# Optimization experiments

Measured on AMD Instinct MI355X. Metric: run time of the kernel, lower is better.

Reference implementation:

```python
import jax, jax.numpy as jnp
import numpy as np

B, N, C = 8, 8192, 256
H = 8            # num_heads
D = C // H       # head dim = 32
P = 64           # proj_size (Linformer rank)


def setup_inputs() -> dict:
    key = jax.random.key(0)
    ks = jax.random.split(key, 12)
    s = lambda fan_in: 1.0 / np.sqrt(fan_in)
    return {
        "x": jax.random.normal(ks[0], (B, N, C), jnp.float32),
        "Wqkvv": jax.random.normal(ks[1], (4 * C, C), jnp.float32) * s(C),
        "WE": jax.random.normal(ks[2], (P, N), jnp.float32) * s(N),
        "bE": jax.random.normal(ks[3], (P,), jnp.float32) * s(N),
        "WF": jax.random.normal(ks[4], (P, N), jnp.float32) * s(N),
        "bF": jax.random.normal(ks[5], (P,), jnp.float32) * s(N),
        "Wo1": jax.random.normal(ks[6], (C // 2, C), jnp.float32) * s(C),
        "bo1": jax.random.normal(ks[7], (C // 2,), jnp.float32) * s(C),
        "Wo2": jax.random.normal(ks[8], (C // 2, C), jnp.float32) * s(C),
        "bo2": jax.random.normal(ks[9], (C // 2,), jnp.float32) * s(C),
        "temp1": jnp.ones((H, 1, 1), jnp.float32),
        "temp2": jnp.ones((H, 1, 1), jnp.float32),
    }


def _l2norm(v, axis=-1, eps=1e-12):
    # matches torch F.normalize
    n = jnp.sqrt(jnp.sum(v * v, axis=axis, keepdims=True))
    return v / jnp.maximum(n, eps)


def reference(x, Wqkvv, WE, bE, WF, bF, Wo1, bo1, Wo2, bo2, temp1, temp2):
    b, n, c = x.shape
    # qkvv: [b,n,4c] -> [4,b,h,d,n]  (includes the .transpose(-2,-1) of each part)
    qkvv = jnp.einsum('bnc,fc->bnf', x, Wqkvv).reshape(b, n, 4, H, D)
    qkvv = qkvv.transpose(2, 0, 3, 4, 1)
    q, k, v_ca, v_sa = qkvv[0], qkvv[1], qkvv[2], qkvv[3]  # each [b,h,d,n]

    # Linformer-style low-rank projections along the token axis
    k_proj = jnp.einsum('bhdn,pn->bhdp', k, WE) + bE   # [b,h,d,p]
    v_proj = jnp.einsum('bhdn,pn->bhdp', v_sa, WF) + bF

    qn = _l2norm(q)
    kn = _l2norm(k)

    # --- channel attention branch (XCiT-style) ---
    attn_ca = jnp.einsum('bhdn,bhen->bhde', qn, kn) * temp1[None]  # [b,h,d,d]
    attn_ca = jax.nn.softmax(attn_ca, axis=-1)  # dropout: eval mode (identity)
    x_ca = jnp.einsum('bhde,bhen->bhdn', attn_ca, v_ca)
    x_ca = x_ca.transpose(0, 3, 1, 2).reshape(b, n, c)  # [b,n,c]

    # --- spatial attention branch (low-rank) ---
    attn_sa = jnp.einsum('bhdn,bhdp->bhnp', qn, k_proj) * temp2[None]  # [b,h,n,p]
    attn_sa = jax.nn.softmax(attn_sa, axis=-1)
    x_sa = jnp.einsum('bhnp,bhdp->bhnd', attn_sa, v_proj)  # [b,h,n,d]
    # faithful to original: permute(0,3,1,2).reshape(b,n,c)
    x_sa = x_sa.transpose(0, 3, 1, 2).reshape(b, n, c)

    x_sa = jnp.einsum('bnc,oc->bno', x_sa, Wo1) + bo1
    x_ca = jnp.einsum('bnc,oc->bno', x_ca, Wo2) + bo2
    return jnp.concatenate((x_sa, x_ca), axis=-1)
```

## Files before the change

kernel.cpp:

```cpp
#include <hip/hip_runtime.h>
#include <hip/hip_bf16.h>
#include <stdint.h>


typedef __attribute__((ext_vector_type(8))) __bf16 bf16x8;
typedef __attribute__((ext_vector_type(4))) __bf16 bf16x4;
typedef __attribute__((ext_vector_type(4))) float f32x4;

#define MFMA(a, b, c) __builtin_amdgcn_mfma_f32_16x16x32_bf16((a), (b), (c), 0, 0, 0)

__device__ __forceinline__ void gl2lds16(const __bf16* g, __bf16* l) {
  __builtin_amdgcn_global_load_lds(
      (const __attribute__((address_space(1))) void*)(const void*)g,
      (__attribute__((address_space(3))) void*)(void*)l, 16, 0, 0);
}

__global__ __launch_bounds__(256) void k_detect(const unsigned short* __restrict__ xr,
                                                int* __restrict__ flag) {
  __shared__ int cnt;
  if (threadIdx.x == 0) cnt = 0;
  __syncthreads();
  int c = 0;
  for (int i = threadIdx.x; i < 8192; i += 256) {
    const int e = (xr[i] >> 7) & 0xFF;
    c += (e >= 0xC0) ? 1 : 0;
  }
  atomicAdd(&cnt, c);
  __syncthreads();
  if (threadIdx.x == 0) *flag = (cnt > 100) ? 1 : 0;
}

__global__ __launch_bounds__(256) void k_convert_x(const void* __restrict__ src,
                                                   __bf16* __restrict__ dst,
                                                   const int* __restrict__ flag) {
  const int i = (blockIdx.x * 256 + threadIdx.x) * 8;
  if (*flag) {
    const float* s = (const float*)src;
    bf16x8 v;
#pragma unroll
    for (int j = 0; j < 8; ++j) v[j] = (__bf16)s[i + j];
    *(bf16x8*)(dst + i) = v;
  } else {
    *(bf16x8*)(dst + i) = *(const bf16x8*)((const __bf16*)src + i);
  }
}

__global__ __launch_bounds__(256) void k_convert_w(
    const void* s0, const void* s1, const void* s2, const void* s3, const void* s4,
    const void* s5, const void* s6, const void* s7, const void* s8, const void* s9,
    const void* s10, __bf16* __restrict__ cw, const int* __restrict__ flag) {
  const int i = (blockIdx.x * 256 + threadIdx.x) * 8;
  if (i >= 1376656) return;
  const void* s;
  int base;
  if (i < 262144)        { s = s0;  base = 0; }
  else if (i < 786432)   { s = s1;  base = 262144; }
  else if (i < 786496)   { s = s2;  base = 786432; }
  else if (i < 1310784)  { s = s3;  base = 786496; }
  else if (i < 1310848)  { s = s4;  base = 1310784; }
  else if (i < 1343616)  { s = s5;  base = 1310848; }
  else if (i < 1343744)  { s = s6;  base = 1343616; }
  else if (i < 1376512)  { s = s7;  base = 1343744; }
  else if (i < 1376640)  { s = s8;  base = 1376512; }
  else if (i < 1376648)  { s = s9;  base = 1376640; }
  else                   { s = s10; base = 1376648; }
  const int li = i - base;
  if (*flag) {
    const float* sf = (const float*)s;
#pragma unroll
    for (int j = 0; j < 8; ++j) cw[i + j] = (__bf16)sf[li + j];
  } else {
    const __bf16* sb = (const __bf16*)s;
#pragma unroll
    for (int j = 0; j < 8; ++j) cw[i + j] = sb[li + j];
  }
}

__global__ __launch_bounds__(256) void k_qkvv(const __bf16* __restrict__ x,
                                              const __bf16* __restrict__ Wq,
                                              __bf16* __restrict__ qkvv) {
  __shared__ alignas(16) __bf16 As[128 * 32];
  __shared__ alignas(16) __bf16 Bs[128 * 32];
  const int t = threadIdx.x, lane = t & 63;
  const int wr = t >> 7, wc = (t >> 6) & 1;
  const int f0 = blockIdx.y * 128;
  const int t0 = blockIdx.x * 128;
  f32x4 acc[4][4] = {};
  const int r = t >> 2, c8 = (t & 3) * 8;
  for (int k0 = 0; k0 < 256; k0 += 32) {
#pragma unroll
    for (int i = 0; i < 2; ++i) {
      gl2lds16(Wq + (size_t)(f0 + i * 64 + r) * 256 + k0 + c8, As + i * 2048 + t * 8);
      gl2lds16(x + (size_t)(t0 + i * 64 + r) * 256 + k0 + c8, Bs + i * 2048 + t * 8);
    }
    __syncthreads();
    bf16x8 af[4], bfr[4];
#pragma unroll
    for (int i = 0; i < 4; ++i) {
      af[i] = *(const bf16x8*)(As + (wr * 64 + i * 16 + (lane & 15)) * 32 + (lane >> 4) * 8);
      bfr[i] = *(const bf16x8*)(Bs + (wc * 64 + i * 16 + (lane & 15)) * 32 + (lane >> 4) * 8);
    }
#pragma unroll
    for (int i = 0; i < 4; ++i)
#pragma unroll
      for (int j = 0; j < 4; ++j) acc[i][j] = MFMA(af[i], bfr[j], acc[i][j]);
    __syncthreads();
  }
  const int b = t0 >> 13;
#pragma unroll
  for (int i = 0; i < 4; ++i) {
#pragma unroll
    for (int j = 0; j < 4; ++j) {
      const int tok = t0 + wc * 64 + j * 16 + (lane & 15);
      const int n = tok & 8191;
#pragma unroll
      for (int rr = 0; rr < 4; ++rr) {
        const int f = f0 + wr * 64 + i * 16 + (lane >> 4) * 4 + rr;
        qkvv[(size_t)(((f >> 8) * 8 + b) * 256 + (f & 255)) * 8192 + n] = (__bf16)acc[i][j][rr];
      }
    }
  }
}

__global__ __launch_bounds__(256) void k_norms(const __bf16* __restrict__ qkvv,
                                               float* __restrict__ qinv,
                                               float* __restrict__ kinv) {
  const int row = blockIdx.x, which = blockIdx.y;
  const __bf16* p = qkvv + (size_t)(which * 2048 + row) * 8192;
  float s = 0.f;
  for (int i = threadIdx.x; i < 8192; i += 256) {
    const float v = (float)p[i];
    s += v * v;
  }
#pragma unroll
  for (int off = 32; off; off >>= 1) s += __shfl_down(s, off, 64);
  __shared__ float red[4];
  if ((threadIdx.x & 63) == 0) red[threadIdx.x >> 6] = s;
  __syncthreads();
  if (threadIdx.x == 0) {
    const float tot = red[0] + red[1] + red[2] + red[3];
    const float inv = 1.0f / fmaxf(sqrtf(tot), 1e-12f);
    (which ? kinv : qinv)[row] = inv;
  }
}

__global__ __launch_bounds__(256) void k_proj_part(const __bf16* __restrict__ qkvv,
                                                   const __bf16* __restrict__ WE,
                                                   const __bf16* __restrict__ WF,
                                                   float* __restrict__ pbuf) {
  __shared__ alignas(16) __bf16 As[128 * 32];
  __shared__ alignas(16) __bf16 Bs[64 * 32];
  const int t = threadIdx.x, lane = t & 63;
  const int wr = t >> 7, wc = (t >> 6) & 1;
  const int kc = blockIdx.x, mt = blockIdx.y, pj = blockIdx.z;
  const __bf16* A = qkvv + (size_t)(pj ? 3 : 1) * 2048 * 8192;
  const __bf16* Bm = pj ? WF : WE;
  const int r0 = mt * 128;
  f32x4 acc[4][2] = {};
  const int r = t >> 2, c8 = (t & 3) * 8;
  for (int k0 = kc * 512; k0 < kc * 512 + 512; k0 += 32) {
#pragma unroll
    for (int i = 0; i < 2; ++i)
      gl2lds16(A + (size_t)(r0 + i * 64 + r) * 8192 + k0 + c8, As + i * 2048 + t * 8);
    gl2lds16(Bm + (size_t)r * 8192 + k0 + c8, Bs + t * 8);
    __syncthreads();
    bf16x8 af[4], bfr[2];
#pragma unroll
    for (int i = 0; i < 4; ++i)
      af[i] = *(const bf16x8*)(As + (wr * 64 + i * 16 + (lane & 15)) * 32 + (lane >> 4) * 8);
#pragma unroll
    for (int j = 0; j < 2; ++j)
      bfr[j] = *(const bf16x8*)(Bs + (wc * 32 + j * 16 + (lane & 15)) * 32 + (lane >> 4) * 8);
#pragma unroll
    for (int i = 0; i < 4; ++i)
#pragma unroll
      for (int j = 0; j < 2; ++j) acc[i][j] = MFMA(af[i], bfr[j], acc[i][j]);
    __syncthreads();
  }
  float* dst = pbuf + (size_t)((pj * 16 + kc) * 2048 + r0) * 64;
#pragma unroll
  for (int i = 0; i < 4; ++i)
#pragma unroll
    for (int j = 0; j < 2; ++j)
#pragma unroll
      for (int rr = 0; rr < 4; ++rr)
        dst[(wr * 64 + i * 16 + (lane >> 4) * 4 + rr) * 64 + wc * 32 + j * 16 + (lane & 15)] =
            acc[i][j][rr];
}

__global__ __launch_bounds__(256) void k_proj_reduce(const float* __restrict__ pbuf,
                                                     const __bf16* __restrict__ bE,
                                                     const __bf16* __restrict__ bF,
                                                     const float* __restrict__ qinv,
                                                     const __bf16* __restrict__ t2,
                                                     __bf16* __restrict__ kprojT,
                                                     __bf16* __restrict__ vprojb) {
  const int idx = blockIdx.x * 256 + threadIdx.x;
  const int pj = idx >> 17, rp = idx & 131071, p = idx & 63;
  const int row = rp >> 6, bh = row >> 5, d = row & 31, h = bh & 7;
  float s = (float)((pj ? bF : bE)[p]);
  const float* src = pbuf + (size_t)pj * 16 * 131072 + rp;
#pragma unroll
  for (int k = 0; k < 16; ++k) s += src[(size_t)k * 131072];
  if (pj == 0)
    kprojT[bh * 2048 + p * 32 + d] = (__bf16)(s * qinv[row] * (float)t2[h]);
  else
    vprojb[bh * 2048 + d * 64 + p] = (__bf16)s;
}

__global__ __launch_bounds__(256) void k_sca_part(const __bf16* __restrict__ qkvv,
                                                  float* __restrict__ spart) {
  const int bh = blockIdx.x, kc = blockIdx.y;
  const int t = threadIdx.x, lane = t & 63, w = t >> 6;
  const __bf16* qb = qkvv + (size_t)(bh * 32) * 8192;
  const __bf16* kb = qkvv + (size_t)(2048 + bh * 32) * 8192;
  f32x4 acc[2][2] = {};
  const int kbase = kc * 1024 + w * 256 + (lane >> 4) * 8;
#pragma unroll
  for (int ks = 0; ks < 256; ks += 32) {
    bf16x8 af[2], bfr[2];
#pragma unroll
    for (int i = 0; i < 2; ++i) {
      af[i] = *(const bf16x8*)(qb + (size_t)(i * 16 + (lane & 15)) * 8192 + kbase + ks);
      bfr[i] = *(const bf16x8*)(kb + (size_t)(i * 16 + (lane & 15)) * 8192 + kbase + ks);
    }
#pragma unroll
    for (int i = 0; i < 2; ++i)
#pragma unroll
      for (int j = 0; j < 2; ++j) acc[i][j] = MFMA(af[i], bfr[j], acc[i][j]);
  }
  float* dst = spart + (size_t)((bh * 8 + kc) * 4 + w) * 1024;
#pragma unroll
  for (int i = 0; i < 2; ++i)
#pragma unroll
    for (int j = 0; j < 2; ++j)
#pragma unroll
      for (int rr = 0; rr < 4; ++rr)
        dst[(i * 16 + (lane >> 4) * 4 + rr) * 32 + j * 16 + (lane & 15)] = acc[i][j][rr];
}

__global__ __launch_bounds__(256) void k_sca_softmax(const float* __restrict__ spart,
                                                     const float* __restrict__ qinv,
                                                     const float* __restrict__ kinv,
                                                     const __bf16* __restrict__ temp1,
                                                     __bf16* __restrict__ attnb) {
  const int bh = blockIdx.x;
  __shared__ float S[1024];
  const int t = threadIdx.x;
  const float tmp = (float)temp1[bh & 7];
  for (int idx = t; idx < 1024; idx += 256) {
    float s = 0.f;
    const float* src = spart + (size_t)bh * 32768 + idx;
#pragma unroll
    for (int k = 0; k < 32; ++k) s += src[k * 1024];
    S[idx] = s * qinv[bh * 32 + (idx >> 5)] * kinv[bh * 32 + (idx & 31)] * tmp;
  }
  __syncthreads();
  const int lane = t & 63, w = t >> 6;
#pragma unroll
  for (int rr = 0; rr < 4; ++rr) {
    const int row = rr * 8 + w * 2 + (lane >> 5);
    const int e = lane & 31;
    float v = S[row * 32 + e];
    float m = v;
#pragma unroll
    for (int off = 16; off; off >>= 1) m = fmaxf(m, __shfl_xor(m, off, 32));
    const float ex = __expf(v - m);
    float sm = ex;
#pragma unroll
    for (int off = 16; off; off >>= 1) sm += __shfl_xor(sm, off, 32);
    attnb[(size_t)bh * 1024 + row * 32 + e] = (__bf16)(ex / sm);
  }
}

__global__ __launch_bounds__(256) void k_ca_mfma(const __bf16* __restrict__ qkvv,
                                                 const __bf16* __restrict__ attnb,
                                                 __bf16* __restrict__ xca) {
  const int t = threadIdx.x, lane = t & 63, w = t >> 6;
  const int l15 = lane & 15, g = lane >> 4;
  const int bh = blockIdx.y, b = bh >> 3, h = bh & 7;
  const __bf16* vb = qkvv + (size_t)(4096 + bh * 32) * 8192;
  bf16x8 aa[2];
#pragma unroll
  for (int mi = 0; mi < 2; ++mi)
    aa[mi] = *(const bf16x8*)(attnb + bh * 1024 + (mi * 16 + l15) * 32 + g * 8);
#pragma unroll
  for (int it = 0; it < 4; ++it) {
    const int n = blockIdx.x * 256 + it * 64 + w * 16 + l15;
    union { bf16x8 v; unsigned short u[8]; } bq;
#pragma unroll
    for (int j = 0; j < 8; ++j)
      bq.u[j] = *(const unsigned short*)(vb + (size_t)(g * 8 + j) * 8192 + n);
    f32x4 o[2] = {};
#pragma unroll
    for (int mi = 0; mi < 2; ++mi) o[mi] = MFMA(aa[mi], bq.v, o[mi]);
#pragma unroll
    for (int mi = 0; mi < 2; ++mi) {
      bf16x4 p4;
#pragma unroll
      for (int rr = 0; rr < 4; ++rr) p4[rr] = (__bf16)o[mi][rr];
      *(bf16x4*)(xca + (size_t)(b * 8192 + n) * 256 + h * 32 + mi * 16 + g * 4) = p4;
    }
  }
}

__global__ __launch_bounds__(256) void k_sa_mfma(const __bf16* __restrict__ qkvv,
                                                 const __bf16* __restrict__ kprojT,
                                                 const __bf16* __restrict__ vprojb,
                                                 __bf16* __restrict__ xsa) {
  __shared__ __bf16 P[4][16 * 72];
  const int t = threadIdx.x, lane = t & 63, w = t >> 6;
  const int l15 = lane & 15, g = lane >> 4;
  const int bh = blockIdx.y;
  const __bf16* qb = qkvv + (size_t)(bh * 32) * 8192;
  bf16x8 ka[4], va[2][2];
#pragma unroll
  for (int tile = 0; tile < 4; ++tile)
    ka[tile] = *(const bf16x8*)(kprojT + bh * 2048 + (tile * 16 + l15) * 32 + g * 8);
#pragma unroll
  for (int mi = 0; mi < 2; ++mi)
#pragma unroll
    for (int kh = 0; kh < 2; ++kh)
      va[mi][kh] = *(const bf16x8*)(vprojb + bh * 2048 + (mi * 16 + l15) * 64 + kh * 32 + g * 8);
  __bf16* Pw = &P[w][0];
#pragma unroll
  for (int it = 0; it < 4; ++it) {
    const int n0 = blockIdx.x * 256 + it * 64 + w * 16;
    union { bf16x8 v; unsigned short u[8]; } bq;
#pragma unroll
    for (int j = 0; j < 8; ++j)
      bq.u[j] = *(const unsigned short*)(qb + (size_t)(g * 8 + j) * 8192 + n0 + l15);
    f32x4 st[4];
#pragma unroll
    for (int tile = 0; tile < 4; ++tile) {
      f32x4 z = {};
      st[tile] = MFMA(ka[tile], bq.v, z);
    }
    float m = st[0][0];
#pragma unroll
    for (int tile = 0; tile < 4; ++tile)
#pragma unroll
      for (int rr = 0; rr < 4; ++rr) m = fmaxf(m, st[tile][rr]);
    m = fmaxf(m, __shfl_xor(m, 16, 64));
    m = fmaxf(m, __shfl_xor(m, 32, 64));
    float sum = 0.f;
#pragma unroll
    for (int tile = 0; tile < 4; ++tile) {
      bf16x4 p4;
#pragma unroll
      for (int rr = 0; rr < 4; ++rr) {
        const float ex = __expf(st[tile][rr] - m);
        sum += ex;
        p4[rr] = (__bf16)ex;
      }
      *(bf16x4*)(Pw + l15 * 72 + tile * 16 + g * 4) = p4;
    }
    sum += __shfl_xor(sum, 16, 64);
    sum += __shfl_xor(sum, 32, 64);
    const float inv = 1.0f / sum;
    f32x4 o[2] = {};
#pragma unroll
    for (int kh = 0; kh < 2; ++kh) {
      const bf16x8 pf = *(const bf16x8*)(Pw + l15 * 72 + kh * 32 + g * 8);
#pragma unroll
      for (int mi = 0; mi < 2; ++mi) o[mi] = MFMA(va[mi][kh], pf, o[mi]);
    }
#pragma unroll
    for (int mi = 0; mi < 2; ++mi)
#pragma unroll
      for (int rr = 0; rr < 4; ++rr) {
        const int d = mi * 16 + g * 4 + rr;
        xsa[(size_t)(bh * 32 + d) * 8192 + n0 + l15] = (__bf16)(o[mi][rr] * inv);
      }
  }
}

__global__ __launch_bounds__(256) void k_out(const __bf16* __restrict__ xsa,
                                             const __bf16* __restrict__ xca,
                                             const __bf16* __restrict__ Wo1,
                                             const __bf16* __restrict__ bo1,
                                             const __bf16* __restrict__ Wo2,
                                             const __bf16* __restrict__ bo2,
                                             void* __restrict__ outv,
                                             const int* __restrict__ flag) {
  __shared__ alignas(16) __bf16 As[128 * 32];
  __shared__ alignas(16) __bf16 Bs[128 * 32];
  const int t = threadIdx.x, lane = t & 63;
  const int wr = t >> 7, wc = (t >> 6) & 1;
  const int nt = blockIdx.x, b = blockIdx.y, br = blockIdx.z;
  const int isf32 = *flag;
  const __bf16* Wo = br ? Wo2 : Wo1;
  const __bf16* bo = br ? bo2 : bo1;
  f32x4 acc[4][4] = {};
  const int r = t >> 2, c8 = (t & 3) * 8;
  for (int k0 = 0; k0 < 256; k0 += 32) {
#pragma unroll
    for (int i = 0; i < 2; ++i) {
      const int row = nt * 128 + i * 64 + r;
      const __bf16* ga;
      if (br == 0) {
        ga = xsa + (size_t)((b * 8 + ((row >> 5) & 7)) * 32 + (row >> 8)) * 8192 +
             (row & 31) * 256 + k0 + c8;
      } else {
        ga = xca + (size_t)(b * 8192 + row) * 256 + k0 + c8;
      }
      gl2lds16(ga, As + i * 2048 + t * 8);
      gl2lds16(Wo + (size_t)(i * 64 + r) * 256 + k0 + c8, Bs + i * 2048 + t * 8);
    }
    __syncthreads();
    bf16x8 af[4], bfr[4];
#pragma unroll
    for (int i = 0; i < 4; ++i) {
      af[i] = *(const bf16x8*)(As + (wr * 64 + i * 16 + (lane & 15)) * 32 + (lane >> 4) * 8);
      bfr[i] = *(const bf16x8*)(Bs + (wc * 64 + i * 16 + (lane & 15)) * 32 + (lane >> 4) * 8);
    }
#pragma unroll
    for (int i = 0; i < 4; ++i)
#pragma unroll
      for (int j = 0; j < 4; ++j) acc[i][j] = MFMA(af[i], bfr[j], acc[i][j]);
    __syncthreads();
  }
  float bias[4];
#pragma unroll
  for (int j = 0; j < 4; ++j) bias[j] = (float)bo[wc * 64 + j * 16 + (lane & 15)];
#pragma unroll
  for (int i = 0; i < 4; ++i) {
#pragma unroll
    for (int j = 0; j < 4; ++j) {
      const int col = wc * 64 + j * 16 + (lane & 15);
#pragma unroll
      for (int rr = 0; rr < 4; ++rr) {
        const int row = nt * 128 + wr * 64 + i * 16 + (lane >> 4) * 4 + rr;
        const float val = acc[i][j][rr] + bias[j];
        const size_t oi = (size_t)(b * 8192 + row) * 256 + br * 128 + col;
        if (isf32) ((float*)outv)[oi] = val;
        else ((__bf16*)outv)[oi] = (__bf16)val;
      }
    }
  }
}

extern "C" void kernel_launch(void* const* d_in, const int* in_sizes, int n_in,
                              void* d_out, int out_size, void* d_ws, size_t ws_size,
                              hipStream_t stream) {
  char* ws = (char*)d_ws;
  __bf16* qkvv   = (__bf16*)(ws);
  __bf16* cinx   = (__bf16*)(ws + 134217728ull);
  __bf16* xca    = (__bf16*)(ws + 134217728ull);
  float*  pbuf   = (float*)(ws + 167772160ull);
  float*  spart  = (float*)(ws + 184549376ull);
  __bf16* xsa    = (__bf16*)(ws + 167772160ull);
  __bf16* kprojT = (__bf16*)(ws + 201326592ull);
  __bf16* vprojb = (__bf16*)(ws + 201588736ull);
  float*  qinv   = (float*)(ws + 201850880ull);
  float*  kinv   = (float*)(ws + 201859072ull);
  __bf16* attnb  = (__bf16*)(ws + 201867264ull);
  __bf16* cw     = (__bf16*)(ws + 201998336ull);
  int*    flag   = (int*)(ws + 204751872ull);

  __bf16* cWq  = cw;
  __bf16* cWE  = cw + 262144;
  __bf16* cbE  = cw + 786432;
  __bf16* cWF  = cw + 786496;
  __bf16* cbF  = cw + 1310784;
  __bf16* cWo1 = cw + 1310848;
  __bf16* cbo1 = cw + 1343616;
  __bf16* cWo2 = cw + 1343744;
  __bf16* cbo2 = cw + 1376512;
  __bf16* ct1  = cw + 1376640;
  __bf16* ct2  = cw + 1376648;

  k_detect<<<1, 256, 0, stream>>>((const unsigned short*)d_in[0], flag);
  k_convert_x<<<8192, 256, 0, stream>>>(d_in[0], cinx, flag);
  k_convert_w<<<673, 256, 0, stream>>>(d_in[1], d_in[2], d_in[3], d_in[4], d_in[5],
                                       d_in[6], d_in[7], d_in[8], d_in[9], d_in[10],
                                       d_in[11], cw, flag);
  k_qkvv<<<dim3(512, 8), 256, 0, stream>>>(cinx, cWq, qkvv);
  k_norms<<<dim3(2048, 2), 256, 0, stream>>>(qkvv, qinv, kinv);
  k_proj_part<<<dim3(16, 16, 2), 256, 0, stream>>>(qkvv, cWE, cWF, pbuf);
  k_proj_reduce<<<dim3(1024), 256, 0, stream>>>(pbuf, cbE, cbF, qinv, ct2, kprojT, vprojb);
  k_sca_part<<<dim3(64, 8), 256, 0, stream>>>(qkvv, spart);
  k_sca_softmax<<<dim3(64), 256, 0, stream>>>(spart, qinv, kinv, ct1, attnb);
  k_ca_mfma<<<dim3(32, 64), 256, 0, stream>>>(qkvv, attnb, xca);
  k_sa_mfma<<<dim3(32, 64), 256, 0, stream>>>(qkvv, kprojT, vprojb, xsa);
  k_out<<<dim3(64, 8, 2), 256, 0, stream>>>(xsa, xca, cWo1, cbo1, cWo2, cbo2, d_out, flag);
}
```

Measured before the change: 332.2 us.

## Fuse norm computation into QKV GEMM, merge attention kernels, swizzle LDS

```diff
diff --git a/kernel.cpp b/kernel.cpp
--- a/kernel.cpp
+++ b/kernel.cpp
@@ -15,26 +15,26 @@
       (__attribute__((address_space(3))) void*)(void*)l, 16, 0, 0);
 }
 
-__global__ __launch_bounds__(256) void k_detect(const unsigned short* __restrict__ xr,
-                                                int* __restrict__ flag) {
-  __shared__ int cnt;
-  if (threadIdx.x == 0) cnt = 0;
-  __syncthreads();
+__device__ __forceinline__ int detect_f32(const unsigned int* __restrict__ xw) {
   int c = 0;
-  for (int i = threadIdx.x; i < 8192; i += 256) {
-    const int e = (xr[i] >> 7) & 0xFF;
-    c += (e >= 0xC0) ? 1 : 0;
-  }
-  atomicAdd(&cnt, c);
-  __syncthreads();
-  if (threadIdx.x == 0) *flag = (cnt > 100) ? 1 : 0;
+#pragma unroll
+  for (int i = 0; i < 64; ++i) {
+    const unsigned int u = xw[i];
+    c += (((u >> 7) & 0xFF) >= 0xC0) ? 1 : 0;
+    c += (((u >> 23) & 0xFF) >= 0xC0) ? 1 : 0;
+  }
+  return c > 8;
 }
 
 __global__ __launch_bounds__(256) void k_convert_x(const void* __restrict__ src,
                                                    __bf16* __restrict__ dst,
-                                                   const int* __restrict__ flag) {
+                                                   float* __restrict__ nsum) {
+  if (blockIdx.x == 0) {
+#pragma unroll
+    for (int j = 0; j < 16; ++j) nsum[threadIdx.x + j * 256] = 0.f;
+  }
   const int i = (blockIdx.x * 256 + threadIdx.x) * 8;
-  if (*flag) {
+  if (detect_f32((const unsigned int*)src)) {
     const float* s = (const float*)src;
     bf16x8 v;
 #pragma unroll
@@ -48,7 +48,7 @@
 __global__ __launch_bounds__(256) void k_convert_w(
     const void* s0, const void* s1, const void* s2, const void* s3, const void* s4,
     const void* s5, const void* s6, const void* s7, const void* s8, const void* s9,
-    const void* s10, __bf16* __restrict__ cw, const int* __restrict__ flag) {
+    const void* s10, __bf16* __restrict__ cw, const void* __restrict__ xsrc) {
   const int i = (blockIdx.x * 256 + threadIdx.x) * 8;
   if (i >= 1376656) return;
   const void* s;
@@ -65,7 +65,7 @@
   else if (i < 1376648)  { s = s9;  base = 1376640; }
   else                   { s = s10; base = 1376648; }
   const int li = i - base;
-  if (*flag) {
+  if (detect_f32((const unsigned int*)xsrc)) {
     const float* sf = (const float*)s;
 #pragma unroll
     for (int j = 0; j < 8; ++j) cw[i + j] = (__bf16)sf[li + j];
@@ -78,15 +78,20 @@
 
 __global__ __launch_bounds__(256) void k_qkvv(const __bf16* __restrict__ x,
                                               const __bf16* __restrict__ Wq,
-                                              __bf16* __restrict__ qkvv) {
+                                              __bf16* __restrict__ qkvv,
+                                              float* __restrict__ qsum,
+                                              float* __restrict__ ksum) {
   __shared__ alignas(16) __bf16 As[128 * 32];
   __shared__ alignas(16) __bf16 Bs[128 * 32];
   const int t = threadIdx.x, lane = t & 63;
   const int wr = t >> 7, wc = (t >> 6) & 1;
+  const int l15 = lane & 15, g = lane >> 4;
   const int f0 = blockIdx.y * 128;
   const int t0 = blockIdx.x * 128;
   f32x4 acc[4][4] = {};
-  const int r = t >> 2, c8 = (t & 3) * 8;
+  const int r = t >> 2;
+  const int c8 = ((t & 3) ^ ((t >> 3) & 3)) * 8;
+  const int cx = ((g ^ ((l15 >> 1) & 3)) * 8);
   for (int k0 = 0; k0 < 256; k0 += 32) {
 #pragma unroll
     for (int i = 0; i < 2; ++i) {
@@ -97,8 +102,8 @@
     bf16x8 af[4], bfr[4];
 #pragma unroll
     for (int i = 0; i < 4; ++i) {
-      af[i] = *(const bf16x8*)(As + (wr * 64 + i * 16 + (lane & 15)) * 32 + (lane >> 4) * 8);
-      bfr[i] = *(const bf16x8*)(Bs + (wc * 64 + i * 16 + (lane & 15)) * 32 + (lane >> 4) * 8);
+      af[i] = *(const bf16x8*)(As + (wr * 64 + i * 16 + l15) * 32 + cx);
+      bfr[i] = *(const bf16x8*)(Bs + (wc * 64 + i * 16 + l15) * 32 + cx);
     }
 #pragma unroll
     for (int i = 0; i < 4; ++i)
@@ -111,36 +116,35 @@
   for (int i = 0; i < 4; ++i) {
 #pragma unroll
     for (int j = 0; j < 4; ++j) {
-      const int tok = t0 + wc * 64 + j * 16 + (lane & 15);
+      const int tok = t0 + wc * 64 + j * 16 + l15;
       const int n = tok & 8191;
 #pragma unroll
       for (int rr = 0; rr < 4; ++rr) {
-        const int f = f0 + wr * 64 + i * 16 + (lane >> 4) * 4 + rr;
+        const int f = f0 + wr * 64 + i * 16 + g * 4 + rr;
         qkvv[(size_t)(((f >> 8) * 8 + b) * 256 + (f & 255)) * 8192 + n] = (__bf16)acc[i][j][rr];
       }
     }
   }
-}
-
-__global__ __launch_bounds__(256) void k_norms(const __bf16* __restrict__ qkvv,
-                                               float* __restrict__ qinv,
-                                               float* __restrict__ kinv) {
-  const int row = blockIdx.x, which = blockIdx.y;
-  const __bf16* p = qkvv + (size_t)(which * 2048 + row) * 8192;
-  float s = 0.f;
-  for (int i = threadIdx.x; i < 8192; i += 256) {
-    const float v = (float)p[i];
-    s += v * v;
-  }
-#pragma unroll
-  for (int off = 32; off; off >>= 1) s += __shfl_down(s, off, 64);
-  __shared__ float red[4];
-  if ((threadIdx.x & 63) == 0) red[threadIdx.x >> 6] = s;
-  __syncthreads();
-  if (threadIdx.x == 0) {
-    const float tot = red[0] + red[1] + red[2] + red[3];
-    const float inv = 1.0f / fmaxf(sqrtf(tot), 1e-12f);
-    (which ? kinv : qinv)[row] = inv;
+  if (f0 < 512) {
+    float* dst = (f0 >> 8) ? ksum : qsum;
+#pragma unroll
+    for (int i = 0; i < 4; ++i) {
+#pragma unroll
+      for (int rr = 0; rr < 4; ++rr) {
+        float s = 0.f;
+#pragma unroll
+        for (int j = 0; j < 4; ++j) {
+          const float v = acc[i][j][rr];
+          s += v * v;
+        }
+#pragma unroll
+        for (int off = 1; off < 16; off <<= 1) s += __shfl_xor(s, off, 16);
+        if (l15 == 0) {
+          const int f = f0 + wr * 64 + i * 16 + g * 4 + rr;
+          atomicAdd(dst + b * 256 + (f & 255), s);
+        }
+      }
+    }
   }
 }
 
@@ -152,12 +156,15 @@
   __shared__ alignas(16) __bf16 Bs[64 * 32];
   const int t = threadIdx.x, lane = t & 63;
   const int wr = t >> 7, wc = (t >> 6) & 1;
+  const int l15 = lane & 15, g = lane >> 4;
   const int kc = blockIdx.x, mt = blockIdx.y, pj = blockIdx.z;
   const __bf16* A = qkvv + (size_t)(pj ? 3 : 1) * 2048 * 8192;
   const __bf16* Bm = pj ? WF : WE;
   const int r0 = mt * 128;
   f32x4 acc[4][2] = {};
-  const int r = t >> 2, c8 = (t & 3) * 8;
+  const int r = t >> 2;
+  const int c8 = ((t & 3) ^ ((t >> 3) & 3)) * 8;
+  const int cx = ((g ^ ((l15 >> 1) & 3)) * 8);
   for (int k0 = kc * 512; k0 < kc * 512 + 512; k0 += 32) {
 #pragma unroll
     for (int i = 0; i < 2; ++i)
@@ -167,10 +174,10 @@
     bf16x8 af[4], bfr[2];
 #pragma unroll
     for (int i = 0; i < 4; ++i)
-      af[i] = *(const bf16x8*)(As + (wr * 64 + i * 16 + (lane & 15)) * 32 + (lane >> 4) * 8);
+      af[i] = *(const bf16x8*)(As + (wr * 64 + i * 16 + l15) * 32 + cx);
 #pragma unroll
     for (int j = 0; j < 2; ++j)
-      bfr[j] = *(const bf16x8*)(Bs + (wc * 32 + j * 16 + (lane & 15)) * 32 + (lane >> 4) * 8);
+      bfr[j] = *(const bf16x8*)(Bs + (wc * 32 + j * 16 + l15) * 32 + cx);
 #pragma unroll
     for (int i = 0; i < 4; ++i)
 #pragma unroll
@@ -184,14 +191,13 @@
     for (int j = 0; j < 2; ++j)
 #pragma unroll
       for (int rr = 0; rr < 4; ++rr)
-        dst[(wr * 64 + i * 16 + (lane >> 4) * 4 + rr) * 64 + wc * 32 + j * 16 + (lane & 15)] =
-            acc[i][j][rr];
+        dst[(wr * 64 + i * 16 + g * 4 + rr) * 64 + wc * 32 + j * 16 + l15] = acc[i][j][rr];
 }
 
 __global__ __launch_bounds__(256) void k_proj_reduce(const float* __restrict__ pbuf,
                                                      const __bf16* __restrict__ bE,
                                                      const __bf16* __restrict__ bF,
-                                                     const float* __restrict__ qinv,
+                                                     const float* __restrict__ qsum,
                                                      const __bf16* __restrict__ t2,
                                                      __bf16* __restrict__ kprojT,
                                                      __bf16* __restrict__ vprojb) {
@@ -202,10 +208,12 @@
   const float* src = pbuf + (size_t)pj * 16 * 131072 + rp;
 #pragma unroll
   for (int k = 0; k < 16; ++k) s += src[(size_t)k * 131072];
-  if (pj == 0)
-    kprojT[bh * 2048 + p * 32 + d] = (__bf16)(s * qinv[row] * (float)t2[h]);
-  else
+  if (pj == 0) {
+    const float qi = 1.0f / fmaxf(sqrtf(qsum[row]), 1e-12f);
+    kprojT[bh * 2048 + p * 32 + d] = (__bf16)(s * qi * (float)t2[h]);
+  } else {
     vprojb[bh * 2048 + d * 64 + p] = (__bf16)s;
+  }
 }
 
 __global__ __launch_bounds__(256) void k_sca_part(const __bf16* __restrict__ qkvv,
@@ -240,8 +248,8 @@
 }
 
 __global__ __launch_bounds__(256) void k_sca_softmax(const float* __restrict__ spart,
-                                                     const float* __restrict__ qinv,
-                                                     const float* __restrict__ kinv,
+                                                     const float* __restrict__ qsum,
+                                                     const float* __restrict__ ksum,
                                                      const __bf16* __restrict__ temp1,
                                                      __bf16* __restrict__ attnb) {
   const int bh = blockIdx.x;
@@ -253,7 +261,9 @@
     const float* src = spart + (size_t)bh * 32768 + idx;
 #pragma unroll
     for (int k = 0; k < 32; ++k) s += src[k * 1024];
-    S[idx] = s * qinv[bh * 32 + (idx >> 5)] * kinv[bh * 32 + (idx & 31)] * tmp;
+    const float qi = 1.0f / fmaxf(sqrtf(qsum[bh * 32 + (idx >> 5)]), 1e-12f);
+    const float ki = 1.0f / fmaxf(sqrtf(ksum[bh * 32 + (idx & 31)]), 1e-12f);
+    S[idx] = s * qi * ki * tmp;
   }
   __syncthreads();
   const int lane = t & 63, w = t >> 6;
@@ -273,105 +283,103 @@
   }
 }
 
-__global__ __launch_bounds__(256) void k_ca_mfma(const __bf16* __restrict__ qkvv,
-                                                 const __bf16* __restrict__ attnb,
-                                                 __bf16* __restrict__ xca) {
-  const int t = threadIdx.x, lane = t & 63, w = t >> 6;
-  const int l15 = lane & 15, g = lane >> 4;
-  const int bh = blockIdx.y, b = bh >> 3, h = bh & 7;
-  const __bf16* vb = qkvv + (size_t)(4096 + bh * 32) * 8192;
-  bf16x8 aa[2];
-#pragma unroll
-  for (int mi = 0; mi < 2; ++mi)
-    aa[mi] = *(const bf16x8*)(attnb + bh * 1024 + (mi * 16 + l15) * 32 + g * 8);
-#pragma unroll
-  for (int it = 0; it < 4; ++it) {
-    const int n = blockIdx.x * 256 + it * 64 + w * 16 + l15;
-    union { bf16x8 v; unsigned short u[8]; } bq;
-#pragma unroll
-    for (int j = 0; j < 8; ++j)
-      bq.u[j] = *(const unsigned short*)(vb + (size_t)(g * 8 + j) * 8192 + n);
-    f32x4 o[2] = {};
-#pragma unroll
-    for (int mi = 0; mi < 2; ++mi) o[mi] = MFMA(aa[mi], bq.v, o[mi]);
-#pragma unroll
-    for (int mi = 0; mi < 2; ++mi) {
-      bf16x4 p4;
-#pragma unroll
-      for (int rr = 0; rr < 4; ++rr) p4[rr] = (__bf16)o[mi][rr];
-      *(bf16x4*)(xca + (size_t)(b * 8192 + n) * 256 + h * 32 + mi * 16 + g * 4) = p4;
-    }
-  }
-}
-
-__global__ __launch_bounds__(256) void k_sa_mfma(const __bf16* __restrict__ qkvv,
-                                                 const __bf16* __restrict__ kprojT,
-                                                 const __bf16* __restrict__ vprojb,
-                                                 __bf16* __restrict__ xsa) {
+__global__ __launch_bounds__(256) void k_casa(const __bf16* __restrict__ qkvv,
+                                              const __bf16* __restrict__ attnb,
+                                              const __bf16* __restrict__ kprojT,
+                                              const __bf16* __restrict__ vprojb,
+                                              __bf16* __restrict__ xca,
+                                              __bf16* __restrict__ xsa) {
   __shared__ __bf16 P[4][16 * 72];
   const int t = threadIdx.x, lane = t & 63, w = t >> 6;
   const int l15 = lane & 15, g = lane >> 4;
-  const int bh = blockIdx.y;
-  const __bf16* qb = qkvv + (size_t)(bh * 32) * 8192;
-  bf16x8 ka[4], va[2][2];
-#pragma unroll
-  for (int tile = 0; tile < 4; ++tile)
-    ka[tile] = *(const bf16x8*)(kprojT + bh * 2048 + (tile * 16 + l15) * 32 + g * 8);
-#pragma unroll
-  for (int mi = 0; mi < 2; ++mi)
-#pragma unroll
-    for (int kh = 0; kh < 2; ++kh)
-      va[mi][kh] = *(const bf16x8*)(vprojb + bh * 2048 + (mi * 16 + l15) * 64 + kh * 32 + g * 8);
-  __bf16* Pw = &P[w][0];
-#pragma unroll
-  for (int it = 0; it < 4; ++it) {
-    const int n0 = blockIdx.x * 256 + it * 64 + w * 16;
-    union { bf16x8 v; unsigned short u[8]; } bq;
-#pragma unroll
-    for (int j = 0; j < 8; ++j)
-      bq.u[j] = *(const unsigned short*)(qb + (size_t)(g * 8 + j) * 8192 + n0 + l15);
-    f32x4 st[4];
-#pragma unroll
-    for (int tile = 0; tile < 4; ++tile) {
-      f32x4 z = {};
-      st[tile] = MFMA(ka[tile], bq.v, z);
-    }
-    float m = st[0][0];
+  if (blockIdx.y < 64) {
+    const int bh = blockIdx.y, b = bh >> 3, h = bh & 7;
+    const __bf16* vb = qkvv + (size_t)(4096 + bh * 32) * 8192;
+    bf16x8 aa[2];
+#pragma unroll
+    for (int mi = 0; mi < 2; ++mi)
+      aa[mi] = *(const bf16x8*)(attnb + bh * 1024 + (mi * 16 + l15) * 32 + g * 8);
+#pragma unroll
+    for (int it = 0; it < 4; ++it) {
+      const int n = blockIdx.x * 256 + it * 64 + w * 16 + l15;
+      union { bf16x8 v; unsigned short u[8]; } bq;
+#pragma unroll
+      for (int j = 0; j < 8; ++j)
+        bq.u[j] = *(const unsigned short*)(vb + (size_t)(g * 8 + j) * 8192 + n);
+      f32x4 o[2] = {};
+#pragma unroll
+      for (int mi = 0; mi < 2; ++mi) o[mi] = MFMA(aa[mi], bq.v, o[mi]);
+#pragma unroll
+      for (int mi = 0; mi < 2; ++mi) {
+        bf16x4 p4;
+#pragma unroll
+        for (int rr = 0; rr < 4; ++rr) p4[rr] = (__bf16)o[mi][rr];
+        *(bf16x4*)(xca + (size_t)(b * 8192 + n) * 256 + h * 32 + mi * 16 + g * 4) = p4;
+      }
+    }
+  } else {
+    const int bh = blockIdx.y - 64;
+    const __bf16* qb = qkvv + (size_t)(bh * 32) * 8192;
+    bf16x8 ka[4], va[2][2];
 #pragma unroll
     for (int tile = 0; tile < 4; ++tile)
-#pragma unroll
-      for (int rr = 0; rr < 4; ++rr) m = fmaxf(m, st[tile][rr]);
-    m = fmaxf(m, __shfl_xor(m, 16, 64));
-    m = fmaxf(m, __shfl_xor(m, 32, 64));
-    float sum = 0.f;
-#pragma unroll
-    for (int tile = 0; tile < 4; ++tile) {
-      bf16x4 p4;
-#pragma unroll
-      for (int rr = 0; rr < 4; ++rr) {
-        const float ex = __expf(st[tile][rr] - m);
-        sum += ex;
-        p4[rr] = (__bf16)ex;
-      }
-      *(bf16x4*)(Pw + l15 * 72 + tile * 16 + g * 4) = p4;
-    }
-    sum += __shfl_xor(sum, 16, 64);
-    sum += __shfl_xor(sum, 32, 64);
-    const float inv = 1.0f / sum;
-    f32x4 o[2] = {};
-#pragma unroll
-    for (int kh = 0; kh < 2; ++kh) {
-      const bf16x8 pf = *(const bf16x8*)(Pw + l15 * 72 + kh * 32 + g * 8);
-#pragma unroll
-      for (int mi = 0; mi < 2; ++mi) o[mi] = MFMA(va[mi][kh], pf, o[mi]);
-    }
+      ka[tile] = *(const bf16x8*)(kprojT + bh * 2048 + (tile * 16 + l15) * 32 + g * 8);
 #pragma unroll
     for (int mi = 0; mi < 2; ++mi)
 #pragma unroll
-      for (int rr = 0; rr < 4; ++rr) {
-        const int d = mi * 16 + g * 4 + rr;
-        xsa[(size_t)(bh * 32 + d) * 8192 + n0 + l15] = (__bf16)(o[mi][rr] * inv);
-      }
+      for (int kh = 0; kh < 2; ++kh)
+        va[mi][kh] = *(const bf16x8*)(vprojb + bh * 2048 + (mi * 16 + l15) * 64 + kh * 32 + g * 8);
+    __bf16* Pw = &P[w][0];
+#pragma unroll
+    for (int it = 0; it < 4; ++it) {
+      const int n0 = blockIdx.x * 256 + it * 64 + w * 16;
+      union { bf16x8 v; unsigned short u[8]; } bq;
+#pragma unroll
+      for (int j = 0; j < 8; ++j)
+        bq.u[j] = *(const unsigned short*)(qb + (size_t)(g * 8 + j) * 8192 + n0 + l15);
+      f32x4 st[4];
+#pragma unroll
+      for (int tile = 0; tile < 4; ++tile) {
+        f32x4 z = {};
+        st[tile] = MFMA(ka[tile], bq.v, z);
+      }
+      float m = st[0][0];
+#pragma unroll
+      for (int tile = 0; tile < 4; ++tile)
+#pragma unroll
+        for (int rr = 0; rr < 4; ++rr) m = fmaxf(m, st[tile][rr]);
+      m = fmaxf(m, __shfl_xor(m, 16, 64));
+      m = fmaxf(m, __shfl_xor(m, 32, 64));
+      float sum = 0.f;
+#pragma unroll
+      for (int tile = 0; tile < 4; ++tile) {
+        bf16x4 p4;
+#pragma unroll
+        for (int rr = 0; rr < 4; ++rr) {
+          const float ex = __expf(st[tile][rr] - m);
+          sum += ex;
+          p4[rr] = (__bf16)ex;
+        }
+        *(bf16x4*)(Pw + l15 * 72 + tile * 16 + g * 4) = p4;
+      }
+      sum += __shfl_xor(sum, 16, 64);
+      sum += __shfl_xor(sum, 32, 64);
+      const float inv = 1.0f / sum;
+      f32x4 o[2] = {};
+#pragma unroll
+      for (int kh = 0; kh < 2; ++kh) {
+        const bf16x8 pf = *(const bf16x8*)(Pw + l15 * 72 + kh * 32 + g * 8);
+#pragma unroll
+        for (int mi = 0; mi < 2; ++mi) o[mi] = MFMA(va[mi][kh], pf, o[mi]);
+      }
+#pragma unroll
+      for (int mi = 0; mi < 2; ++mi)
+#pragma unroll
+        for (int rr = 0; rr < 4; ++rr) {
+          const int d = mi * 16 + g * 4 + rr;
+          xsa[(size_t)(bh * 32 + d) * 8192 + n0 + l15] = (__bf16)(o[mi][rr] * inv);
+        }
+    }
   }
 }
 
@@ -382,17 +390,20 @@
                                              const __bf16* __restrict__ Wo2,
                                              const __bf16* __restrict__ bo2,
                                              void* __restrict__ outv,
-                                             const int* __restrict__ flag) {
+                                             const void* __restrict__ xsrc) {
   __shared__ alignas(16) __bf16 As[128 * 32];
   __shared__ alignas(16) __bf16 Bs[128 * 32];
   const int t = threadIdx.x, lane = t & 63;
   const int wr = t >> 7, wc = (t >> 6) & 1;
+  const int l15 = lane & 15, g = lane >> 4;
   const int nt = blockIdx.x, b = blockIdx.y, br = blockIdx.z;
-  const int isf32 = *flag;
+  const int isf32 = detect_f32((const unsigned int*)xsrc);
   const __bf16* Wo = br ? Wo2 : Wo1;
   const __bf16* bo = br ? bo2 : bo1;
   f32x4 acc[4][4] = {};
-  const int r = t >> 2, c8 = (t & 3) * 8;
+  const int r = t >> 2;
+  const int c8 = ((t & 3) ^ ((t >> 3) & 3)) * 8;
+  const int cx = ((g ^ ((l15 >> 1) & 3)) * 8);
   for (int k0 = 0; k0 < 256; k0 += 32) {
 #pragma unroll
     for (int i = 0; i < 2; ++i) {
@@ -411,8 +422,8 @@
     bf16x8 af[4], bfr[4];
 #pragma unroll
     for (int i = 0; i < 4; ++i) {
-      af[i] = *(const bf16x8*)(As + (wr * 64 + i * 16 + (lane & 15)) * 32 + (lane >> 4) * 8);
-      bfr[i] = *(const bf16x8*)(Bs + (wc * 64 + i * 16 + (lane & 15)) * 32 + (lane >> 4) * 8);
+      af[i] = *(const bf16x8*)(As + (wr * 64 + i * 16 + l15) * 32 + cx);
+      bfr[i] = *(const bf16x8*)(Bs + (wc * 64 + i * 16 + l15) * 32 + cx);
     }
 #pragma unroll
     for (int i = 0; i < 4; ++i)
@@ -422,15 +433,15 @@
   }
   float bias[4];
 #pragma unroll
-  for (int j = 0; j < 4; ++j) bias[j] = (float)bo[wc * 64 + j * 16 + (lane & 15)];
+  for (int j = 0; j < 4; ++j) bias[j] = (float)bo[wc * 64 + j * 16 + l15];
 #pragma unroll
   for (int i = 0; i < 4; ++i) {
 #pragma unroll
     for (int j = 0; j < 4; ++j) {
-      const int col = wc * 64 + j * 16 + (lane & 15);
+      const int col = wc * 64 + j * 16 + l15;
 #pragma unroll
       for (int rr = 0; rr < 4; ++rr) {
-        const int row = nt * 128 + wr * 64 + i * 16 + (lane >> 4) * 4 + rr;
+        const int row = nt * 128 + wr * 64 + i * 16 + g * 4 + rr;
         const float val = acc[i][j][rr] + bias[j];
         const size_t oi = (size_t)(b * 8192 + row) * 256 + br * 128 + col;
         if (isf32) ((float*)outv)[oi] = val;
@@ -452,11 +463,10 @@
   __bf16* xsa    = (__bf16*)(ws + 167772160ull);
   __bf16* kprojT = (__bf16*)(ws + 201326592ull);
   __bf16* vprojb = (__bf16*)(ws + 201588736ull);
-  float*  qinv   = (float*)(ws + 201850880ull);
-  float*  kinv   = (float*)(ws + 201859072ull);
+  float*  qsum   = (float*)(ws + 201850880ull);
+  float*  ksum   = (float*)(ws + 201859072ull);
   __bf16* attnb  = (__bf16*)(ws + 201867264ull);
   __bf16* cw     = (__bf16*)(ws + 201998336ull);
-  int*    flag   = (int*)(ws + 204751872ull);
 
   __bf16* cWq  = cw;
   __bf16* cWE  = cw + 262144;
@@ -470,18 +480,15 @@
   __bf16* ct1  = cw + 1376640;
   __bf16* ct2  = cw + 1376648;
 
-  k_detect<<<1, 256, 0, stream>>>((const unsigned short*)d_in[0], flag);
-  k_convert_x<<<8192, 256, 0, stream>>>(d_in[0], cinx, flag);
+  k_convert_x<<<8192, 256, 0, stream>>>(d_in[0], cinx, qsum);
   k_convert_w<<<673, 256, 0, stream>>>(d_in[1], d_in[2], d_in[3], d_in[4], d_in[5],
                                        d_in[6], d_in[7], d_in[8], d_in[9], d_in[10],
-                                       d_in[11], cw, flag);
-  k_qkvv<<<dim3(512, 8), 256, 0, stream>>>(cinx, cWq, qkvv);
-  k_norms<<<dim3(2048, 2), 256, 0, stream>>>(qkvv, qinv, kinv);
+                                       d_in[11], cw, d_in[0]);
+  k_qkvv<<<dim3(512, 8), 256, 0, stream>>>(cinx, cWq, qkvv, qsum, ksum);
   k_proj_part<<<dim3(16, 16, 2), 256, 0, stream>>>(qkvv, cWE, cWF, pbuf);
-  k_proj_reduce<<<dim3(1024), 256, 0, stream>>>(pbuf, cbE, cbF, qinv, ct2, kprojT, vprojb);
+  k_proj_reduce<<<dim3(1024), 256, 0, stream>>>(pbuf, cbE, cbF, qsum, ct2, kprojT, vprojb);
   k_sca_part<<<dim3(64, 8), 256, 0, stream>>>(qkvv, spart);
-  k_sca_softmax<<<dim3(64), 256, 0, stream>>>(spart, qinv, kinv, ct1, attnb);
-  k_ca_mfma<<<dim3(32, 64), 256, 0, stream>>>(qkvv, attnb, xca);
-  k_sa_mfma<<<dim3(32, 64), 256, 0, stream>>>(qkvv, kprojT, vprojb, xsa);
-  k_out<<<dim3(64, 8, 2), 256, 0, stream>>>(xsa, xca, cWo1, cbo1, cWo2, cbo2, d_out, flag);
-}
+  k_sca_softmax<<<dim3(64), 256, 0, stream>>>(spart, qsum, ksum, ct1, attnb);
+  k_casa<<<dim3(32, 128), 256, 0, stream>>>(qkvv, attnb, kprojT, vprojb, xca, xsa);
+  k_out<<<dim3(64, 8, 2), 256, 0, stream>>>(xsa, xca, cWo1, cbo1, cWo2, cbo2, d_out, d_in[0]);
+}
```

Measured after the change: 330.0 us. No clear change (-0.7%).
